# Kernel optimization log

Hardware: AMD Instinct MI355X
Metric: run time of the kernel (lower is better)

The kernel has to match this reference:

```python
import jax, jax.numpy as jnp
import numpy as np

N_NODES = 100000
N_EDGES = 1600000
IN_DIM, HID_DIM, OUT_DIM = 128, 128, 1


def gcn_conv(x, W, b, src, dst, n_nodes):
    """PyG-style GCNConv: add self-loops, symmetric D^-1/2 (A+I) D^-1/2 normalization.

    x: [N, F_in], W: [F_in, F_out], b: [F_out], src/dst: [E] int edge endpoints.
    """
    h = x @ W  # [N, F_out] transform first (as PyG does)
    # degree on A + I, counted over destination (symmetric graph assumption)
    ones = jnp.ones(src.shape[0], dtype=h.dtype)
    deg = jax.ops.segment_sum(ones, dst, num_segments=n_nodes) + 1.0  # +1 self loop
    dinv = jax.lax.rsqrt(deg)  # [N]
    norm = dinv[src] * dinv[dst]  # [E] edge normalization
    msg = h[src] * norm[:, None]  # [E, F_out] gather + scale
    agg = jax.ops.segment_sum(msg, dst, num_segments=n_nodes)  # scatter-add
    # self-loop contribution: norm_ii = dinv[i]^2
    out = agg + h * (dinv * dinv)[:, None]
    return out + b


def setup_inputs() -> dict:
    key = jax.random.key(0)
    k1, k2, k3, k4 = jax.random.split(key, 4)
    x = jax.random.normal(k1, (N_NODES, IN_DIM), dtype=jnp.float32)
    edge_index = jax.random.randint(k2, (2, N_EDGES), 0, N_NODES, dtype=jnp.int64)
    W1 = jax.random.normal(k3, (IN_DIM, HID_DIM), dtype=jnp.float32) * (1.0 / np.sqrt(IN_DIM))
    b1 = jnp.zeros((HID_DIM,), dtype=jnp.float32)
    W2 = jax.random.normal(k4, (HID_DIM, OUT_DIM), dtype=jnp.float32) * (1.0 / np.sqrt(HID_DIM))
    b2 = jnp.zeros((OUT_DIM,), dtype=jnp.float32)
    return {"x": x, "edge_index": edge_index, "W1": W1, "b1": b1, "W2": W2, "b2": b2}


def reference(x, edge_index, W1, b1, W2, b2):
    n = x.shape[0]
    src, dst = edge_index[0], edge_index[1]
    h = gcn_conv(x, W1, b1, src, dst, n)
    h = jax.nn.relu(h)
    # dropout(p=0.2) is identity at inference
    out = gcn_conv(h, W2, b2, src, dst, n)  # [N, 1]
    return out
```

## Files before the change

kernel.cpp:

```cpp
#include <hip/hip_runtime.h>

#define N_NODES 100000
#define N_EDGES 1600000
#define DIM 128

#define BSHIFT 8
#define BNODES 256
#define NBUCK 391
#define BCAP  4608
#define PCHUNK 4096
#define NB_PART ((N_EDGES + PCHUNK - 1) / PCHUNK)

#define GTILES 1563
#define GGRID  1563

typedef short s16x8 __attribute__((ext_vector_type(8)));
typedef float f32x4 __attribute__((ext_vector_type(4)));

__device__ __forceinline__ unsigned short f2bf(float f) {
    unsigned u = __float_as_uint(f);
    u += 0x7fffu + ((u >> 16) & 1u);
    return (unsigned short)(u >> 16);
}
__device__ __forceinline__ float bflo(unsigned u) { return __uint_as_float(u << 16); }
__device__ __forceinline__ float bfhi(unsigned u) { return __uint_as_float(u & 0xffff0000u); }

__device__ __forceinline__ void acc8(float (&a)[8], uint4 v, float w) {
    a[0] = fmaf(bflo(v.x), w, a[0]); a[1] = fmaf(bfhi(v.x), w, a[1]);
    a[2] = fmaf(bflo(v.y), w, a[2]); a[3] = fmaf(bfhi(v.y), w, a[3]);
    a[4] = fmaf(bflo(v.z), w, a[4]); a[5] = fmaf(bfhi(v.z), w, a[5]);
    a[6] = fmaf(bflo(v.w), w, a[6]); a[7] = fmaf(bfhi(v.w), w, a[7]);
}


__global__ void k_zero(int* __restrict__ gcur) {
    int t = blockIdx.x * blockDim.x + threadIdx.x;
    if (t < NBUCK) gcur[t] = t * BCAP;
}

__device__ __forceinline__ void part_body(char* smem, int bid,
                                          const int* __restrict__ src,
                                          const int* __restrict__ dst,
                                          int* __restrict__ gcur,
                                          int2* __restrict__ ebuf) {
    int* hist = (int*)smem;
    int* gbase = hist + NBUCK;
    int tid = threadIdx.x;
    long e0 = (long)bid * PCHUNK;
    int n = min(PCHUNK, (int)(N_EDGES - e0));
    for (int b = tid; b < NBUCK; b += 256) hist[b] = 0;
    __syncthreads();

    int mys[16], myd[16];
#pragma unroll
    for (int k = 0; k < 16; ++k) {
        int idx = k * 256 + tid;
        if (idx < n) {
            mys[k] = src[e0 + idx];
            myd[k] = dst[e0 + idx];
            atomicAdd(&hist[myd[k] >> BSHIFT], 1);
        } else {
            myd[k] = -1;
        }
    }
    __syncthreads();
    for (int b = tid; b < NBUCK; b += 256) {
        gbase[b] = hist[b] ? atomicAdd(&gcur[b], hist[b]) : 0;
        hist[b] = 0;
    }
    __syncthreads();
#pragma unroll
    for (int k = 0; k < 16; ++k) {
        if (myd[k] >= 0) {
            int b = myd[k] >> BSHIFT;
            int slot = gbase[b] + atomicAdd(&hist[b], 1);
            ebuf[slot] = make_int2(mys[k], myd[k]);
        }
    }
}

__device__ __forceinline__ void gemm_body(char* smem, int bid,
                                          const float* __restrict__ x,
                                          const float* __restrict__ W1,
                                          unsigned short* __restrict__ h1) {
    unsigned short* Wt = (unsigned short*)smem;
    int tid = threadIdx.x;
    for (int idx = tid; idx < DIM * DIM; idx += 256) {
        int k = idx >> 7, c = idx & 127;
        Wt[c * 128 + (k ^ ((c & 7) << 3))] = f2bf(W1[idx]);
    }
    __syncthreads();

    int wv = tid >> 6, lane = tid & 63;
    int g = lane >> 4, tl = lane & 15;
    unsigned short* cst = (unsigned short*)(smem + 32768 + wv * 4096);

    for (int tile = bid; tile < GTILES; tile += GGRID) {
        int rb = tile * 64 + wv * 16;
        if (rb >= N_NODES) continue;

        s16x8 afrag[4];
        const float* xrow = x + (size_t)(rb + tl) * DIM + g * 8;
#pragma unroll
        for (int kc = 0; kc < 4; ++kc) {
            float4 p0 = *(const float4*)(xrow + kc * 32);
            float4 p1 = *(const float4*)(xrow + kc * 32 + 4);
            s16x8 a;
            a[0] = (short)f2bf(p0.x); a[1] = (short)f2bf(p0.y);
            a[2] = (short)f2bf(p0.z); a[3] = (short)f2bf(p0.w);
            a[4] = (short)f2bf(p1.x); a[5] = (short)f2bf(p1.y);
            a[6] = (short)f2bf(p1.z); a[7] = (short)f2bf(p1.w);
            afrag[kc] = a;
        }

        f32x4 acc[8];
#pragma unroll
        for (int ct = 0; ct < 8; ++ct) acc[ct] = (f32x4)0.0f;
#pragma unroll
        for (int kc = 0; kc < 4; ++kc) {
#pragma unroll
            for (int ct = 0; ct < 8; ++ct) {
                int crow = ct * 16 + tl;
                int boff = crow * 256 + ((kc * 64 + g * 16) ^ ((crow & 7) << 4));
                s16x8 b = *(const s16x8*)((const char*)Wt + boff);
                acc[ct] = __builtin_amdgcn_mfma_f32_16x16x32_bf16(afrag[kc], b, acc[ct], 0, 0, 0);
            }
        }

#pragma unroll
        for (int ct = 0; ct < 8; ++ct) {
#pragma unroll
            for (int r = 0; r < 4; ++r) {
                float own = acc[ct][r];
                float oth = __shfl_xor(own, 1, 64);
                if ((lane & 1) == 0) {
                    unsigned pk = (unsigned)f2bf(own) | ((unsigned)f2bf(oth) << 16);
                    int row = g * 4 + r;
                    int col = ct * 16 + tl;
                    *(unsigned*)&cst[row * 128 + (col ^ (row << 3))] = pk;
                }
            }
        }
        asm volatile("s_waitcnt lgkmcnt(0)" ::: "memory");

        unsigned short* dstp = h1 + (size_t)rb * DIM;
#pragma unroll
        for (int c = 0; c < 4; ++c) {
            int row = c * 4 + g;
            uint4 v = *(const uint4*)&cst[row * 128 + ((tl ^ row) * 8)];
            *(uint4*)(dstp + c * 512 + lane * 8) = v;
        }
    }
}

__global__ __launch_bounds__(256) void k_part(const int* __restrict__ src,
                                              const int* __restrict__ dst,
                                              int* __restrict__ gcur,
                                              int2* __restrict__ ebuf) {
    __shared__ __align__(16) char smem[2 * NBUCK * 4 + 16];
    part_body(smem, blockIdx.x, src, dst, gcur, ebuf);
}

__global__ __launch_bounds__(256) void k_gemm(const float* __restrict__ x,
                                              const float* __restrict__ W1,
                                              unsigned short* __restrict__ h1) {
    __shared__ __align__(16) char smem[49152];
    gemm_body(smem, blockIdx.x, x, W1, h1);
}

__global__ __launch_bounds__(256) void k_pg(const int* __restrict__ src,
                                            const int* __restrict__ dst,
                                            int* __restrict__ gcur,
                                            int2* __restrict__ ebuf,
                                            const float* __restrict__ x,
                                            const float* __restrict__ W1,
                                            unsigned short* __restrict__ h1) {
    __shared__ __align__(16) char smem[49152];
    if (blockIdx.x < NB_PART) part_body(smem, blockIdx.x, src, dst, gcur, ebuf);
    else                      gemm_body(smem, blockIdx.x - NB_PART, x, W1, h1);
}

__global__ __launch_bounds__(256) void k_csr(const int2* __restrict__ ebuf,
                                             const int* __restrict__ gcur,
                                             int* __restrict__ rp,
                                             int* __restrict__ cnt,
                                             float* __restrict__ dinv,
                                             int* __restrict__ csrs) {
    __shared__ int lcnt[BNODES];
    __shared__ int lcur[BNODES];
    int b = blockIdx.x, t = threadIdx.x;
    int node0 = b << BSHIFT;
    lcnt[t] = 0;
    __syncthreads();
    int base = b * BCAP, end = gcur[b];
    for (int e = base + t; e < end; e += 256)
        atomicAdd(&lcnt[ebuf[e].y - node0], 1);
    __syncthreads();
    int c = lcnt[t];
    lcur[t] = c;
    __syncthreads();
    for (int s = 1; s < 256; s <<= 1) {
        int u = (t >= s) ? lcur[t - s] : 0;
        __syncthreads();
        lcur[t] += u;
        __syncthreads();
    }
    int excl = lcur[t] - c;
    lcur[t] = excl;
    int node = node0 + t;
    if (node < N_NODES) {
        rp[node] = base + excl;
        cnt[node] = c;
        dinv[node] = rsqrtf((float)(c + 1));
    }
    __syncthreads();
    for (int e = base + t; e < end; e += 256) {
        int2 d = ebuf[e];
        int p = atomicAdd(&lcur[d.y - node0], 1);
        csrs[base + p] = d.x;
    }
}


__global__ __launch_bounds__(256) void k_agg1(const unsigned short* __restrict__ h1,
                                              const float* __restrict__ dinv,
                                              const int* __restrict__ rp,
                                              const int* __restrict__ cnt,
                                              const int* __restrict__ csrs,
                                              const float* __restrict__ b1,
                                              const float* __restrict__ W2,
                                              float* __restrict__ z) {
    int lane = threadIdx.x & 63;
    int wv = threadIdx.x >> 6;
    int g = lane >> 4, tl = lane & 15;
    int i = blockIdx.x * 16 + wv * 4 + g;
    int c0 = tl * 8;
    float di = dinv[i];
    int beg = rp[i], end = beg + cnt[i];
    float a[8];
#pragma unroll
    for (int q = 0; q < 8; ++q) a[q] = 0.f;
    const unsigned short* hbase = h1 + c0;

    int j = beg;
    for (; j + 4 <= end; j += 4) {
        int s0 = csrs[j], s1 = csrs[j + 1], s2 = csrs[j + 2], s3 = csrs[j + 3];
        uint4 v0 = *(const uint4*)(hbase + (size_t)s0 * DIM);
        uint4 v1 = *(const uint4*)(hbase + (size_t)s1 * DIM);
        uint4 v2 = *(const uint4*)(hbase + (size_t)s2 * DIM);
        uint4 v3 = *(const uint4*)(hbase + (size_t)s3 * DIM);
        float w0 = dinv[s0] * di, w1 = dinv[s1] * di;
        float w2 = dinv[s2] * di, w3 = dinv[s3] * di;
        acc8(a, v0, w0);
        acc8(a, v1, w1);
        acc8(a, v2, w2);
        acc8(a, v3, w3);
    }
    for (; j < end; ++j) {
        int s0 = csrs[j];
        uint4 v0 = *(const uint4*)(hbase + (size_t)s0 * DIM);
        acc8(a, v0, dinv[s0] * di);
    }

    uint4 vs = *(const uint4*)(hbase + (size_t)i * DIM);
    float sii = di * di;
    float4 bA = *(const float4*)(b1 + c0);
    float4 bB = *(const float4*)(b1 + c0 + 4);
    float4 wA = *(const float4*)(W2 + c0);
    float4 wB = *(const float4*)(W2 + c0 + 4);
    float p = 0.f;
    p += fmaxf(fmaf(bflo(vs.x), sii, a[0]) + bA.x, 0.f) * wA.x;
    p += fmaxf(fmaf(bfhi(vs.x), sii, a[1]) + bA.y, 0.f) * wA.y;
    p += fmaxf(fmaf(bflo(vs.y), sii, a[2]) + bA.z, 0.f) * wA.z;
    p += fmaxf(fmaf(bfhi(vs.y), sii, a[3]) + bA.w, 0.f) * wA.w;
    p += fmaxf(fmaf(bflo(vs.z), sii, a[4]) + bB.x, 0.f) * wB.x;
    p += fmaxf(fmaf(bfhi(vs.z), sii, a[5]) + bB.y, 0.f) * wB.y;
    p += fmaxf(fmaf(bflo(vs.w), sii, a[6]) + bB.z, 0.f) * wB.z;
    p += fmaxf(fmaf(bfhi(vs.w), sii, a[7]) + bB.w, 0.f) * wB.w;
#pragma unroll
    for (int off = 8; off >= 1; off >>= 1) p += __shfl_xor(p, off, 64);
    if (tl == 0) z[i] = p;
}


__global__ __launch_bounds__(256) void k_agg2(const float* __restrict__ zin,
                                              const float* __restrict__ dinv,
                                              const int* __restrict__ rp,
                                              const int* __restrict__ cnt,
                                              const int* __restrict__ csrs,
                                              const float* __restrict__ b2,
                                              float* __restrict__ out) {
    int i = blockIdx.x * blockDim.x + threadIdx.x;
    if (i >= N_NODES) return;
    float di = dinv[i];
    int beg = rp[i], end = beg + cnt[i];
    float acc = 0.f;
    int j = beg;
    for (; j + 4 <= end; j += 4) {
        int s0 = csrs[j], s1 = csrs[j + 1], s2 = csrs[j + 2], s3 = csrs[j + 3];
        float z0 = zin[s0], z1 = zin[s1], z2 = zin[s2], z3 = zin[s3];
        acc = fmaf(z0, dinv[s0] * di, acc);
        acc = fmaf(z1, dinv[s1] * di, acc);
        acc = fmaf(z2, dinv[s2] * di, acc);
        acc = fmaf(z3, dinv[s3] * di, acc);
    }
    for (; j < end; ++j) {
        int s0 = csrs[j];
        acc = fmaf(zin[s0], dinv[s0] * di, acc);
    }
    out[i] = acc + zin[i] * di * di + b2[0];
}


extern "C" void kernel_launch(void* const* d_in, const int* in_sizes, int n_in,
                              void* d_out, int out_size, void* d_ws, size_t ws_size,
                              hipStream_t stream) {
    const float* x  = (const float*)d_in[0];
    const int*   ei = (const int*)d_in[1];
    const float* W1 = (const float*)d_in[2];
    const float* b1 = (const float*)d_in[3];
    const float* W2 = (const float*)d_in[4];
    const float* b2 = (const float*)d_in[5];
    float* out = (float*)d_out;

    const int* src = ei;
    const int* dst = ei + N_EDGES;

    char* ws = (char*)d_ws;
    size_t o = 0;
    auto take = [&](size_t bytes) { char* p = ws + o; o += (bytes + 255) & ~(size_t)255; return p; };
    int*   cnt   = (int*)take(sizeof(int) * N_NODES);
    int*   rp    = (int*)take(sizeof(int) * N_NODES);
    int*   gcur  = (int*)take(sizeof(int) * (NBUCK + 1));
    float* dinv  = (float*)take(sizeof(float) * N_NODES);
    float* z     = (float*)take(sizeof(float) * N_NODES);
    int*   csrs  = (int*)take(sizeof(int) * (size_t)NBUCK * BCAP);
    unsigned short* h1 = (unsigned short*)take(sizeof(unsigned short) * (size_t)N_NODES * DIM);
    int2* ebuf_sep = (int2*)take(sizeof(int2) * (size_t)NBUCK * BCAP);
    bool fused = (o <= ws_size);
    int2* ebuf = fused ? ebuf_sep : (int2*)h1;

    const int NB_N = (N_NODES + 255) / 256;

    k_zero<<<2, 256, 0, stream>>>(gcur);
    if (fused) {
        k_pg<<<NB_PART + GGRID, 256, 0, stream>>>(src, dst, gcur, ebuf, x, W1, h1);
        k_csr<<<NBUCK, 256, 0, stream>>>(ebuf, gcur, rp, cnt, dinv, csrs);
    } else {
        k_part<<<NB_PART, 256, 0, stream>>>(src, dst, gcur, ebuf);
        k_csr<<<NBUCK, 256, 0, stream>>>(ebuf, gcur, rp, cnt, dinv, csrs);
        k_gemm<<<GGRID, 256, 0, stream>>>(x, W1, h1);
    }
    k_agg1<<<N_NODES / 16, 256, 0, stream>>>(h1, dinv, rp, cnt, csrs, b1, W2, z);
    k_agg2<<<NB_N, 256, 0, stream>>>(z, dinv, rp, cnt, csrs, b2, out);
}
```

Measured before the change: 142.1 us.

## Split h1 into column halves for cache-friendly aggregation and rebalance GEMM across kernels

Stores the bf16 hidden features as two separate 64-column halves so each layer-1 aggregation block gathers from a 12.8 MB half-array, which can improve cache hit rates for random neighbour gathers. Aggregation now runs per half, writes partial dot products, and a new reduction kernel sums them. The GEMM tiles are also split between the partition kernel and the CSR build kernel so the CSR build overlaps with part of the GEMM. The cost is re-reading the CSR indices and dinv twice, plus an extra launch and partial buffer.

Measured after the change: 141.8 us. Within noise of the previous version (-0.2%).

```diff
diff --git a/kernel.cpp b/kernel.cpp
--- a/kernel.cpp
+++ b/kernel.cpp
@@ -12,7 +12,9 @@
 #define NB_PART ((N_EDGES + PCHUNK - 1) / PCHUNK)
 
 #define GTILES 1563
-#define GGRID  1563
+#define GHALF  625
+
+#define HALF_ELEMS ((size_t)N_NODES * 64)
 
 typedef short s16x8 __attribute__((ext_vector_type(8)));
 typedef float f32x4 __attribute__((ext_vector_type(4)));
@@ -79,116 +81,16 @@
     }
 }
 
-__device__ __forceinline__ void gemm_body(char* smem, int bid,
-                                          const float* __restrict__ x,
-                                          const float* __restrict__ W1,
-                                          unsigned short* __restrict__ h1) {
-    unsigned short* Wt = (unsigned short*)smem;
-    int tid = threadIdx.x;
-    for (int idx = tid; idx < DIM * DIM; idx += 256) {
-        int k = idx >> 7, c = idx & 127;
-        Wt[c * 128 + (k ^ ((c & 7) << 3))] = f2bf(W1[idx]);
-    }
-    __syncthreads();
-
-    int wv = tid >> 6, lane = tid & 63;
-    int g = lane >> 4, tl = lane & 15;
-    unsigned short* cst = (unsigned short*)(smem + 32768 + wv * 4096);
-
-    for (int tile = bid; tile < GTILES; tile += GGRID) {
-        int rb = tile * 64 + wv * 16;
-        if (rb >= N_NODES) continue;
-
-        s16x8 afrag[4];
-        const float* xrow = x + (size_t)(rb + tl) * DIM + g * 8;
-#pragma unroll
-        for (int kc = 0; kc < 4; ++kc) {
-            float4 p0 = *(const float4*)(xrow + kc * 32);
-            float4 p1 = *(const float4*)(xrow + kc * 32 + 4);
-            s16x8 a;
-            a[0] = (short)f2bf(p0.x); a[1] = (short)f2bf(p0.y);
-            a[2] = (short)f2bf(p0.z); a[3] = (short)f2bf(p0.w);
-            a[4] = (short)f2bf(p1.x); a[5] = (short)f2bf(p1.y);
-            a[6] = (short)f2bf(p1.z); a[7] = (short)f2bf(p1.w);
-            afrag[kc] = a;
-        }
-
-        f32x4 acc[8];
-#pragma unroll
-        for (int ct = 0; ct < 8; ++ct) acc[ct] = (f32x4)0.0f;
-#pragma unroll
-        for (int kc = 0; kc < 4; ++kc) {
-#pragma unroll
-            for (int ct = 0; ct < 8; ++ct) {
-                int crow = ct * 16 + tl;
-                int boff = crow * 256 + ((kc * 64 + g * 16) ^ ((crow & 7) << 4));
-                s16x8 b = *(const s16x8*)((const char*)Wt + boff);
-                acc[ct] = __builtin_amdgcn_mfma_f32_16x16x32_bf16(afrag[kc], b, acc[ct], 0, 0, 0);
-            }
-        }
-
-#pragma unroll
-        for (int ct = 0; ct < 8; ++ct) {
-#pragma unroll
-            for (int r = 0; r < 4; ++r) {
-                float own = acc[ct][r];
-                float oth = __shfl_xor(own, 1, 64);
-                if ((lane & 1) == 0) {
-                    unsigned pk = (unsigned)f2bf(own) | ((unsigned)f2bf(oth) << 16);
-                    int row = g * 4 + r;
-                    int col = ct * 16 + tl;
-                    *(unsigned*)&cst[row * 128 + (col ^ (row << 3))] = pk;
-                }
-            }
-        }
-        asm volatile("s_waitcnt lgkmcnt(0)" ::: "memory");
-
-        unsigned short* dstp = h1 + (size_t)rb * DIM;
-#pragma unroll
-        for (int c = 0; c < 4; ++c) {
-            int row = c * 4 + g;
-            uint4 v = *(const uint4*)&cst[row * 128 + ((tl ^ row) * 8)];
-            *(uint4*)(dstp + c * 512 + lane * 8) = v;
-        }
-    }
-}
-
-__global__ __launch_bounds__(256) void k_part(const int* __restrict__ src,
-                                              const int* __restrict__ dst,
-                                              int* __restrict__ gcur,
-                                              int2* __restrict__ ebuf) {
-    __shared__ __align__(16) char smem[2 * NBUCK * 4 + 16];
-    part_body(smem, blockIdx.x, src, dst, gcur, ebuf);
-}
-
-__global__ __launch_bounds__(256) void k_gemm(const float* __restrict__ x,
-                                              const float* __restrict__ W1,
-                                              unsigned short* __restrict__ h1) {
-    __shared__ __align__(16) char smem[49152];
-    gemm_body(smem, blockIdx.x, x, W1, h1);
-}
-
-__global__ __launch_bounds__(256) void k_pg(const int* __restrict__ src,
-                                            const int* __restrict__ dst,
-                                            int* __restrict__ gcur,
-                                            int2* __restrict__ ebuf,
-                                            const float* __restrict__ x,
-                                            const float* __restrict__ W1,
-                                            unsigned short* __restrict__ h1) {
-    __shared__ __align__(16) char smem[49152];
-    if (blockIdx.x < NB_PART) part_body(smem, blockIdx.x, src, dst, gcur, ebuf);
-    else                      gemm_body(smem, blockIdx.x - NB_PART, x, W1, h1);
-}
-
-__global__ __launch_bounds__(256) void k_csr(const int2* __restrict__ ebuf,
-                                             const int* __restrict__ gcur,
-                                             int* __restrict__ rp,
-                                             int* __restrict__ cnt,
-                                             float* __restrict__ dinv,
-                                             int* __restrict__ csrs) {
-    __shared__ int lcnt[BNODES];
-    __shared__ int lcur[BNODES];
-    int b = blockIdx.x, t = threadIdx.x;
+__device__ __forceinline__ void csr_body(char* smem, int b,
+                                         const int2* __restrict__ ebuf,
+                                         const int* __restrict__ gcur,
+                                         int* __restrict__ rp,
+                                         int* __restrict__ cnt,
+                                         float* __restrict__ dinv,
+                                         int* __restrict__ csrs) {
+    int* lcnt = (int*)smem;
+    int* lcur = lcnt + BNODES;
+    int t = threadIdx.x;
     int node0 = b << BSHIFT;
     lcnt[t] = 0;
     __syncthreads();
@@ -221,34 +123,160 @@
     }
 }
 
-
-__global__ __launch_bounds__(256) void k_agg1(const unsigned short* __restrict__ h1,
-                                              const float* __restrict__ dinv,
-                                              const int* __restrict__ rp,
-                                              const int* __restrict__ cnt,
-                                              const int* __restrict__ csrs,
-                                              const float* __restrict__ b1,
-                                              const float* __restrict__ W2,
-                                              float* __restrict__ z) {
+__device__ __forceinline__ void gemm_body(char* smem, int tile,
+                                          const float* __restrict__ x,
+                                          const float* __restrict__ W1,
+                                          unsigned short* __restrict__ h1h) {
+    if (tile >= GTILES) return;
+    unsigned short* Wt = (unsigned short*)smem;
+    int tid = threadIdx.x;
+    for (int idx = tid; idx < DIM * DIM; idx += 256) {
+        int k = idx >> 7, c = idx & 127;
+        Wt[c * 128 + (k ^ ((c & 7) << 3))] = f2bf(W1[idx]);
+    }
+    __syncthreads();
+
+    int wv = tid >> 6, lane = tid & 63;
+    int g = lane >> 4, tl = lane & 15;
+    unsigned short* cst = (unsigned short*)(smem + 32768 + wv * 4096);
+
+    int rb = tile * 64 + wv * 16;
+    if (rb >= N_NODES) return;
+
+    s16x8 afrag[4];
+    const float* xrow = x + (size_t)(rb + tl) * DIM + g * 8;
+#pragma unroll
+    for (int kc = 0; kc < 4; ++kc) {
+        float4 p0 = *(const float4*)(xrow + kc * 32);
+        float4 p1 = *(const float4*)(xrow + kc * 32 + 4);
+        s16x8 a;
+        a[0] = (short)f2bf(p0.x); a[1] = (short)f2bf(p0.y);
+        a[2] = (short)f2bf(p0.z); a[3] = (short)f2bf(p0.w);
+        a[4] = (short)f2bf(p1.x); a[5] = (short)f2bf(p1.y);
+        a[6] = (short)f2bf(p1.z); a[7] = (short)f2bf(p1.w);
+        afrag[kc] = a;
+    }
+
+    f32x4 acc[8];
+#pragma unroll
+    for (int ct = 0; ct < 8; ++ct) acc[ct] = (f32x4)0.0f;
+#pragma unroll
+    for (int kc = 0; kc < 4; ++kc) {
+#pragma unroll
+        for (int ct = 0; ct < 8; ++ct) {
+            int crow = ct * 16 + tl;
+            int boff = crow * 256 + ((kc * 64 + g * 16) ^ ((crow & 7) << 4));
+            s16x8 b = *(const s16x8*)((const char*)Wt + boff);
+            acc[ct] = __builtin_amdgcn_mfma_f32_16x16x32_bf16(afrag[kc], b, acc[ct], 0, 0, 0);
+        }
+    }
+
+#pragma unroll
+    for (int ct = 0; ct < 8; ++ct) {
+#pragma unroll
+        for (int r = 0; r < 4; ++r) {
+            float own = acc[ct][r];
+            float oth = __shfl_xor(own, 1, 64);
+            if ((lane & 1) == 0) {
+                unsigned pk = (unsigned)f2bf(own) | ((unsigned)f2bf(oth) << 16);
+                int row = g * 4 + r;
+                int col = ct * 16 + tl;
+                *(unsigned*)&cst[row * 128 + (col ^ (row << 3))] = pk;
+            }
+        }
+    }
+    asm volatile("s_waitcnt lgkmcnt(0)" ::: "memory");
+
+    int hf = tl >> 3, ch = (tl & 7) * 8;
+#pragma unroll
+    for (int c = 0; c < 4; ++c) {
+        int row = c * 4 + g;
+        uint4 v = *(const uint4*)&cst[row * 128 + ((tl ^ row) * 8)];
+        *(uint4*)(h1h + (size_t)hf * HALF_ELEMS + (size_t)(rb + row) * 64 + ch) = v;
+    }
+}
+
+__global__ __launch_bounds__(256) void k_part(const int* __restrict__ src,
+                                              const int* __restrict__ dst,
+                                              int* __restrict__ gcur,
+                                              int2* __restrict__ ebuf) {
+    __shared__ __align__(16) char smem[2 * NBUCK * 4 + 16];
+    part_body(smem, blockIdx.x, src, dst, gcur, ebuf);
+}
+
+__global__ __launch_bounds__(256) void k_gemm(const float* __restrict__ x,
+                                              const float* __restrict__ W1,
+                                              unsigned short* __restrict__ h1h) {
+    __shared__ __align__(16) char smem[49152];
+    gemm_body(smem, blockIdx.x, x, W1, h1h);
+}
+
+__global__ __launch_bounds__(256) void k_csrk(const int2* __restrict__ ebuf,
+                                              const int* __restrict__ gcur,
+                                              int* __restrict__ rp,
+                                              int* __restrict__ cnt,
+                                              float* __restrict__ dinv,
+                                              int* __restrict__ csrs) {
+    __shared__ __align__(16) char smem[2 * BNODES * 4];
+    csr_body(smem, blockIdx.x, ebuf, gcur, rp, cnt, dinv, csrs);
+}
+
+__global__ __launch_bounds__(256) void k_pg1(const int* __restrict__ src,
+                                             const int* __restrict__ dst,
+                                             int* __restrict__ gcur,
+                                             int2* __restrict__ ebuf,
+                                             const float* __restrict__ x,
+                                             const float* __restrict__ W1,
+                                             unsigned short* __restrict__ h1h) {
+    __shared__ __align__(16) char smem[49152];
+    if (blockIdx.x < NB_PART) part_body(smem, blockIdx.x, src, dst, gcur, ebuf);
+    else                      gemm_body(smem, blockIdx.x - NB_PART, x, W1, h1h);
+}
+
+__global__ __launch_bounds__(256) void k_pg2(const int2* __restrict__ ebuf,
+                                             const int* __restrict__ gcur,
+                                             int* __restrict__ rp,
+                                             int* __restrict__ cnt,
+                                             float* __restrict__ dinv,
+                                             int* __restrict__ csrs,
+                                             const float* __restrict__ x,
+                                             const float* __restrict__ W1,
+                                             unsigned short* __restrict__ h1h) {
+    __shared__ __align__(16) char smem[49152];
+    if (blockIdx.x < NBUCK) csr_body(smem, blockIdx.x, ebuf, gcur, rp, cnt, dinv, csrs);
+    else                    gemm_body(smem, GHALF + (blockIdx.x - NBUCK), x, W1, h1h);
+}
+
+
+__global__ __launch_bounds__(256) void k_agg1h(const unsigned short* __restrict__ h1h,
+                                               const float* __restrict__ dinv,
+                                               const int* __restrict__ rp,
+                                               const int* __restrict__ cnt,
+                                               const int* __restrict__ csrs,
+                                               const float* __restrict__ b1,
+                                               const float* __restrict__ W2,
+                                               float* __restrict__ zpart) {
+    int half = blockIdx.x & 1;
+    int nb = blockIdx.x >> 1;
     int lane = threadIdx.x & 63;
     int wv = threadIdx.x >> 6;
-    int g = lane >> 4, tl = lane & 15;
-    int i = blockIdx.x * 16 + wv * 4 + g;
+    int g = lane >> 3, tl = lane & 7;
+    int i = nb * 32 + wv * 8 + g;
     int c0 = tl * 8;
+    const unsigned short* hbase = h1h + (size_t)half * HALF_ELEMS + c0;
     float di = dinv[i];
     int beg = rp[i], end = beg + cnt[i];
     float a[8];
 #pragma unroll
     for (int q = 0; q < 8; ++q) a[q] = 0.f;
-    const unsigned short* hbase = h1 + c0;
 
     int j = beg;
     for (; j + 4 <= end; j += 4) {
         int s0 = csrs[j], s1 = csrs[j + 1], s2 = csrs[j + 2], s3 = csrs[j + 3];
-        uint4 v0 = *(const uint4*)(hbase + (size_t)s0 * DIM);
-        uint4 v1 = *(const uint4*)(hbase + (size_t)s1 * DIM);
-        uint4 v2 = *(const uint4*)(hbase + (size_t)s2 * DIM);
-        uint4 v3 = *(const uint4*)(hbase + (size_t)s3 * DIM);
+        uint4 v0 = *(const uint4*)(hbase + (size_t)s0 * 64);
+        uint4 v1 = *(const uint4*)(hbase + (size_t)s1 * 64);
+        uint4 v2 = *(const uint4*)(hbase + (size_t)s2 * 64);
+        uint4 v3 = *(const uint4*)(hbase + (size_t)s3 * 64);
         float w0 = dinv[s0] * di, w1 = dinv[s1] * di;
         float w2 = dinv[s2] * di, w3 = dinv[s3] * di;
         acc8(a, v0, w0);
@@ -258,16 +286,17 @@
     }
     for (; j < end; ++j) {
         int s0 = csrs[j];
-        uint4 v0 = *(const uint4*)(hbase + (size_t)s0 * DIM);
+        uint4 v0 = *(const uint4*)(hbase + (size_t)s0 * 64);
         acc8(a, v0, dinv[s0] * di);
     }
 
-    uint4 vs = *(const uint4*)(hbase + (size_t)i * DIM);
+    uint4 vs = *(const uint4*)(hbase + (size_t)i * 64);
     float sii = di * di;
-    float4 bA = *(const float4*)(b1 + c0);
-    float4 bB = *(const float4*)(b1 + c0 + 4);
-    float4 wA = *(const float4*)(W2 + c0);
-    float4 wB = *(const float4*)(W2 + c0 + 4);
+    int cb = half * 64 + c0;
+    float4 bA = *(const float4*)(b1 + cb);
+    float4 bB = *(const float4*)(b1 + cb + 4);
+    float4 wA = *(const float4*)(W2 + cb);
+    float4 wB = *(const float4*)(W2 + cb + 4);
     float p = 0.f;
     p += fmaxf(fmaf(bflo(vs.x), sii, a[0]) + bA.x, 0.f) * wA.x;
     p += fmaxf(fmaf(bfhi(vs.x), sii, a[1]) + bA.y, 0.f) * wA.y;
@@ -278,8 +307,13 @@
     p += fmaxf(fmaf(bflo(vs.w), sii, a[6]) + bB.z, 0.f) * wB.z;
     p += fmaxf(fmaf(bfhi(vs.w), sii, a[7]) + bB.w, 0.f) * wB.w;
 #pragma unroll
-    for (int off = 8; off >= 1; off >>= 1) p += __shfl_xor(p, off, 64);
-    if (tl == 0) z[i] = p;
+    for (int off = 4; off >= 1; off >>= 1) p += __shfl_xor(p, off, 64);
+    if (tl == 0) zpart[(size_t)half * N_NODES + i] = p;
+}
+
+__global__ void k_zred(const float* __restrict__ zpart, float* __restrict__ z) {
+    int i = blockIdx.x * blockDim.x + threadIdx.x;
+    if (i < N_NODES) z[i] = zpart[i] + zpart[N_NODES + i];
 }
 
 
@@ -334,23 +368,25 @@
     int*   gcur  = (int*)take(sizeof(int) * (NBUCK + 1));
     float* dinv  = (float*)take(sizeof(float) * N_NODES);
     float* z     = (float*)take(sizeof(float) * N_NODES);
+    float* zpart = (float*)take(sizeof(float) * 2 * N_NODES);
     int*   csrs  = (int*)take(sizeof(int) * (size_t)NBUCK * BCAP);
-    unsigned short* h1 = (unsigned short*)take(sizeof(unsigned short) * (size_t)N_NODES * DIM);
+    unsigned short* h1h = (unsigned short*)take(sizeof(unsigned short) * 2 * HALF_ELEMS);
     int2* ebuf_sep = (int2*)take(sizeof(int2) * (size_t)NBUCK * BCAP);
     bool fused = (o <= ws_size);
-    int2* ebuf = fused ? ebuf_sep : (int2*)h1;
+    int2* ebuf = fused ? ebuf_sep : (int2*)h1h;
 
     const int NB_N = (N_NODES + 255) / 256;
 
     k_zero<<<2, 256, 0, stream>>>(gcur);
     if (fused) {
-        k_pg<<<NB_PART + GGRID, 256, 0, stream>>>(src, dst, gcur, ebuf, x, W1, h1);
-        k_csr<<<NBUCK, 256, 0, stream>>>(ebuf, gcur, rp, cnt, dinv, csrs);
+        k_pg1<<<NB_PART + GHALF, 256, 0, stream>>>(src, dst, gcur, ebuf, x, W1, h1h);
+        k_pg2<<<NBUCK + (GTILES - GHALF), 256, 0, stream>>>(ebuf, gcur, rp, cnt, dinv, csrs, x, W1, h1h);
     } else {
         k_part<<<NB_PART, 256, 0, stream>>>(src, dst, gcur, ebuf);
-        k_csr<<<NBUCK, 256, 0, stream>>>(ebuf, gcur, rp, cnt, dinv, csrs);
-        k_gemm<<<GGRID, 256, 0, stream>>>(x, W1, h1);
-    }
-    k_agg1<<<N_NODES / 16, 256, 0, stream>>>(h1, dinv, rp, cnt, csrs, b1, W2, z);
+        k_csrk<<<NBUCK, 256, 0, stream>>>(ebuf, gcur, rp, cnt, dinv, csrs);
+        k_gemm<<<GTILES, 256, 0, stream>>>(x, W1, h1h);
+    }
+    k_agg1h<<<2 * (N_NODES / 32), 256, 0, stream>>>(h1h, dinv, rp, cnt, csrs, b1, W2, zpart);
+    k_zred<<<NB_N, 256, 0, stream>>>(zpart, z);
     k_agg2<<<NB_N, 256, 0, stream>>>(z, dinv, rp, cnt, csrs, b2, out);
 }
```
